# Performance work log

Measured on AMD Instinct MI355X. Metric: run time of the kernel, lower is better.

Reference implementation:

```python
import jax, jax.numpy as jnp
import numpy as np

NB, NC = 100000, 10000   # buildings, communities
EB, EC = 400000, 80000   # edges
BD, CD = 64, 32          # feature dims


def _glorot(key, shape):
    fan_in = shape[-2] if len(shape) > 1 else shape[0]
    return jax.random.normal(key, shape, jnp.float32) * (1.0 / np.sqrt(fan_in))


def setup_inputs() -> dict:
    key = jax.random.key(0)
    ks = iter(jax.random.split(key, 40))
    inp = {}
    inp['building_features'] = jax.random.normal(next(ks), (NB, BD), jnp.float32)
    inp['community_features'] = jax.random.normal(next(ks), (NC, CD), jnp.float32)
    inp['building_edge_index'] = jax.random.randint(next(ks), (2, EB), 0, NB, jnp.int32)
    inp['community_edge_index'] = jax.random.randint(next(ks), (2, EC), 0, NC, jnp.int32)
    inp['building_to_comm_mapping'] = jax.random.randint(next(ks), (NB,), 0, NC, jnp.int32)
    inp['c1_wl'] = _glorot(next(ks), (CD, 512)); inp['c1_wr'] = _glorot(next(ks), (CD, 512))
    inp['c1_att'] = _glorot(next(ks), (8, 64)); inp['c1_b'] = jnp.zeros((512,), jnp.float32)
    inp['c2_wl'] = _glorot(next(ks), (512, 128)); inp['c2_wr'] = _glorot(next(ks), (512, 128))
    inp['c2_att'] = _glorot(next(ks), (4, 32)); inp['c2_b'] = jnp.zeros((128,), jnp.float32)
    # feature attention: 8 heads of MLP (64+128)->128->2
    inp['fa_w1'] = _glorot(next(ks), (8, BD + 128, 128)); inp['fa_b1'] = jnp.zeros((8, 128), jnp.float32)
    inp['fa_w2'] = _glorot(next(ks), (8, 128, 2)); inp['fa_b2'] = jnp.zeros((8, 2), jnp.float32)
    inp['b1_wl'] = _glorot(next(ks), (BD + 128, 512)); inp['b1_wr'] = _glorot(next(ks), (BD + 128, 512))
    inp['b1_att'] = _glorot(next(ks), (8, 64)); inp['b1_b'] = jnp.zeros((512,), jnp.float32)
    inp['b2_wl'] = _glorot(next(ks), (512, 128)); inp['b2_wr'] = _glorot(next(ks), (512, 128))
    inp['b2_att'] = _glorot(next(ks), (4, 32)); inp['b2_b'] = jnp.zeros((128,), jnp.float32)
    inp['b3_wl'] = _glorot(next(ks), (128, 2)); inp['b3_wr'] = _glorot(next(ks), (128, 2))
    inp['b3_att'] = _glorot(next(ks), (1, 2)); inp['b3_b'] = jnp.zeros((2,), jnp.float32)
    return inp


def gatv2(x, src, dst, wl, wr, att, b, heads, out_dim, concat=True):
    """PyG GATv2Conv (eval mode, self-loops already appended to src/dst)."""
    n = x.shape[0]
    xl = (x @ wl).reshape(n, heads, out_dim)  # source transform
    xr = (x @ wr).reshape(n, heads, out_dim)  # target transform
    e = jax.nn.leaky_relu(xl[src] + xr[dst], 0.2)          # [E,H,D]
    logits = jnp.einsum('ehd,hd->eh', e, att)              # [E,H]
    m = jax.ops.segment_max(logits, dst, num_segments=n)   # stable softmax per target
    p = jnp.exp(logits - m[dst])
    denom = jax.ops.segment_sum(p, dst, num_segments=n)
    alpha = p / denom[dst]
    agg = jax.ops.segment_sum(alpha[:, :, None] * xl[src], dst, num_segments=n)
    agg = agg.reshape(n, heads * out_dim) if concat else agg.mean(axis=1)
    return agg + b


def _with_self_loops(edge_index, n):
    loops = jnp.arange(n, dtype=edge_index.dtype)
    return (jnp.concatenate([edge_index[0], loops]), jnp.concatenate([edge_index[1], loops]))


def _forward(building_features, community_features,
             c1_wl, c1_wr, c1_att, c1_b, c2_wl, c2_wr, c2_att, c2_b,
             fa_w1, fa_b1, fa_w2, fa_b2,
             b1_wl, b1_wr, b1_att, b1_b, b2_wl, b2_wr, b2_att, b2_b,
             b3_wl, b3_wr, b3_att, b3_b,
             building_edge_index, community_edge_index, building_to_comm_mapping):
    csrc, cdst = _with_self_loops(community_edge_index, NC)
    bsrc, bdst = _with_self_loops(building_edge_index, NB)
    # community GNN (dropout is identity in eval)
    cx = jax.nn.relu(gatv2(community_features, csrc, cdst, c1_wl, c1_wr, c1_att, c1_b, 8, 64))
    cx = jax.nn.relu(gatv2(cx, csrc, cdst, c2_wl, c2_wr, c2_att, c2_b, 4, 32))  # [NC,128]
    bcf = cx[building_to_comm_mapping]                                          # [NB,128]
    # multi-head feature attention fusion (vectorized over 8 heads)
    combined = jnp.concatenate([building_features, bcf], axis=1)                # [NB,192]
    h = jax.nn.relu(jnp.einsum('nf,hfk->nhk', combined, fa_w1) + fa_b1)         # [NB,8,128]
    w = jax.nn.softmax(jnp.einsum('nhk,hko->nho', h, fa_w2) + fa_b2, axis=-1)   # [NB,8,2]
    wmean = w.mean(axis=1)                                                      # mean over heads == mean of weighted copies
    fused = jnp.concatenate([building_features * wmean[:, 0:1], bcf * wmean[:, 1:2]], axis=1)
    # building GNN (single batched graph == Batch.from_data_list over all communities)
    x = jax.nn.relu(gatv2(fused, bsrc, bdst, b1_wl, b1_wr, b1_att, b1_b, 8, 64))
    x = jax.nn.relu(gatv2(x, bsrc, bdst, b2_wl, b2_wr, b2_att, b2_b, 4, 32))
    x = gatv2(x, bsrc, bdst, b3_wl, b3_wr, b3_att, b3_b, 1, 2)                   # [NB,2]
    return jax.nn.log_softmax(x, axis=1)


def reference(building_features, community_features,
              c1_wl, c1_wr, c1_att, c1_b, c2_wl, c2_wr, c2_att, c2_b,
              fa_w1, fa_b1, fa_w2, fa_b2,
              b1_wl, b1_wr, b1_att, b1_b, b2_wl, b2_wr, b2_att, b2_b,
              b3_wl, b3_wr, b3_att, b3_b,
              building_edge_index, community_edge_index, building_to_comm_mapping):
    return _forward(building_features, community_features,
                    c1_wl, c1_wr, c1_att, c1_b, c2_wl, c2_wr, c2_att, c2_b,
                    fa_w1, fa_b1, fa_w2, fa_b2,
                    b1_wl, b1_wr, b1_att, b1_b, b2_wl, b2_wr, b2_att, b2_b,
                    b3_wl, b3_wr, b3_att, b3_b,
                    building_edge_index, community_edge_index, building_to_comm_mapping)
```

## Files before the change

kernel.cpp:

```cpp
#include <hip/hip_runtime.h>

static constexpr int NBLD = 100000, NCOM = 10000, EBU = 400000, ECO = 80000;
static constexpr int EBT = EBU + NBLD;
static constexpr int ECT = ECO + NCOM;

typedef _Float16 f16;
typedef _Float16 f16x2 __attribute__((ext_vector_type(2)));
typedef _Float16 f16x8 __attribute__((ext_vector_type(8)));
typedef float f32x4 __attribute__((ext_vector_type(4)));

static constexpr size_t OFF_X1H  = 0;
static constexpr size_t OFF_CXL  = 0;
static constexpr size_t OFF_CXR  = 10240000;
static constexpr size_t OFF_CX1  = 20480000;
static constexpr size_t OFF_CX2L = 30720000;
static constexpr size_t OFF_CX2R = 33280000;
static constexpr size_t OFF_X2   = 0;
static constexpr size_t OFF_XLH  = 102400000;
static constexpr size_t OFF_XRH  = 128000000;
static constexpr size_t OFF_XL2  = 102400000;
static constexpr size_t OFF_XR2  = 128000000;
static constexpr size_t OFF_BF16 = 153600000;
static constexpr size_t OFF_CXF16= 166400000;
static constexpr size_t OFF_WM   = 168960000;
// ... 67 lines not shown
  int e = blockIdx.x * blockDim.x + threadIdx.x;
  if (e < EBT) {
    int dst = (e < EBU) ? bdst[e] : (e - EBU);
    atomicAdd(&bcnt[dst], 1);
  } else {
    int e2 = e - EBT;
    if (e2 >= ECT) return;
    int dst = (e2 < ECO) ? cdst[e2] : (e2 - ECO);
    atomicAdd(&ccnt[dst], 1);
  }
}

__global__ void k_scan1g(const int* __restrict__ bcnt, const int* __restrict__ ccnt,
                         int* __restrict__ boff, int* __restrict__ coff,
                         int* __restrict__ bsum, int* __restrict__ csum) {
  const int* cnt = blockIdx.y ? ccnt : bcnt;
  int* off = blockIdx.y ? coff : boff;
  int* sum = blockIdx.y ? csum : bsum;
  int N = blockIdx.y ? NCOM : NBLD;
  __shared__ int sh[256];
  int tid = threadIdx.x;
  int base = blockIdx.x * 2048 + tid * 8;
  int c[8]; int s = 0;
#pragma unroll
  for (int j = 0; j < 8; ++j) { int i = base + j; c[j] = (i < N) ? cnt[i] : 0; s += c[j]; }
  sh[tid] = s; __syncthreads();
  int own = s;
  for (int o = 1; o < 256; o <<= 1) {
    int v = (tid >= o) ? sh[tid - o] : 0; __syncthreads();
    sh[tid] += v; __syncthreads();
  }
  int ex = sh[tid] - own;
#pragma unroll
  for (int j = 0; j < 8; ++j) { int i = base + j; if (i < N) off[i] = ex; ex += c[j]; }
  if (tid == 255) sum[blockIdx.x] = sh[255];
}

__global__ void k_scan2g(const int* __restrict__ bsum, const int* __restrict__ csum,
                         int nb, int nc, int* __restrict__ bpre, int* __restrict__ cpre) {
  const int* sum = blockIdx.x ? csum : bsum;
  int n = blockIdx.x ? nc : nb;
  int* pre = blockIdx.x ? cpre : bpre;
  __shared__ int sh[256];
  int tid = threadIdx.x;
  int v0 = (tid < n) ? sum[tid] : 0;
  sh[tid] = v0; __syncthreads();
  for (int o = 1; o < 256; o <<= 1) {
    int v = (tid >= o) ? sh[tid - o] : 0; __syncthreads();
    sh[tid] += v; __syncthreads();
  }
  pre[tid] = sh[tid] - v0;
}

__global__ void k_scan3c(int* __restrict__ off, int N, const int* __restrict__ bpre, int Et,
                         int* __restrict__ cur) {
  int i = blockIdx.x * blockDim.x + threadIdx.x;
  if (i < N) {
    int v = off[i] + bpre[i >> 11];
    off[i] = v;
    cur[i] = v;
  }
  if (i == 0) off[N] = Et;
}

__global__ void k_scatter2(const int* __restrict__ bsrc, const int* __restrict__ bdst,
                           const int* __restrict__ csrc, const int* __restrict__ cdst,
                           int* __restrict__ bcur, int* __restrict__ ccur,
                           int* __restrict__ bout, int* __restrict__ cout) {
  int e = blockIdx.x * blockDim.x + threadIdx.x;
  if (e < EBT) {
    int s, d;
    if (e < EBU) { s = bsrc[e]; d = bdst[e]; } else { s = d = e - EBU; }
    bout[atomicAdd(&bcur[d], 1)] = s;
  } else {
    int e2 = e - EBT;
    if (e2 >= ECT) return;
    int s, d;
    if (e2 < ECO) { s = csrc[e2]; d = cdst[e2]; } else { s = d = e2 - ECO; }
    cout[atomicAdd(&ccur[d], 1)] = s;
  }
}


struct frag32 { f16x8 v0, v1; };

static __device__ inline frag32 loadA_lin(const f16* __restrict__ X, int lda,
                                          int k0, int tid, int bm, int M) {
  int row = tid >> 1, half = tid & 1;
  int grow = bm + row;
  frag32 r; r.v0 = (f16x8){}; r.v1 = (f16x8){};
  if (grow < M) {
    const f16* p = X + (size_t)grow * lda + k0 + half * 16;
    r.v0 = *(const f16x8*)(p);
    r.v1 = *(const f16x8*)(p + 8);
  }
  return r;
}

template<bool SCALE>
static __device__ inline frag32 loadA_fused(const f16* __restrict__ bf16h,
                                            const f16* __restrict__ cx16, int mrow,
                                            f16 s0, f16 s1, int k0, int tid, int grow, int M) {
  int half = tid & 1;
  int gc = k0 + half * 16;
  frag32 r; r.v0 = (f16x8){}; r.v1 = (f16x8){};
  if (grow < M) {
    const f16* src; f16 s;
    if (gc < 64) { src = bf16h + (size_t)grow * 64 + gc; s = s0; }
    else         { src = cx16 + (size_t)mrow * 128 + (gc - 64); s = s1; }
    r.v0 = *(const f16x8*)(src);
    r.v1 = *(const f16x8*)(src + 8);
    if (SCALE) {
#pragma unroll
      for (int j = 0; j < 8; ++j) { r.v0[j] *= s; r.v1[j] *= s; }
    }
  }
  return r;
}

static __device__ inline frag32 loadB_T(const f16* __restrict__ WT, int ldk, int k0, int tid) {
  int col = tid >> 1, half = tid & 1;
  const f16* p = WT + (size_t)col * ldk + k0 + half * 16;
  frag32 r;
  r.v0 = *(const f16x8*)(p);
  r.v1 = *(const f16x8*)(p + 8);
  return r;
}

static __device__ inline frag32 loadB_Tpair(const f16* __restrict__ WLt, const f16* __restrict__ WRt,
                                            int ldk, int slab, int k0, int tid) {
  int col = tid >> 1, half = tid & 1;
  const f16* base = (col < 64) ? (WLt + (size_t)(slab + col) * ldk)
                               : (WRt + (size_t)(slab + col - 64) * ldk);
  const f16* p = base + k0 + half * 16;
  frag32 r;
  r.v0 = *(const f16x8*)(p);
  r.v1 = *(const f16x8*)(p + 8);
  return r;
}

static __device__ inline void writeFrag(f16 (*S)[40], frag32 f, int tid) {
  int row = tid >> 1, half = tid & 1;
  *(f16x8*)&S[row][half * 16]     = f.v0;
  *(f16x8*)&S[row][half * 16 + 8] = f.v1;
}

static __device__ inline void mma_tiles(const f16 (*As)[40], const f16 (*Bs)[40],
                                        f32x4 acc[4][4], int wm, int wn, int lane) {
  int rl = lane & 15;
  int kg = (lane >> 4) * 8;
  f16x8 a[4], b[4];
#pragma unroll
  for (int i = 0; i < 4; ++i) a[i] = *(const f16x8*)&As[wm * 64 + i * 16 + rl][kg];
#pragma unroll
  for (int j = 0; j < 4; ++j) b[j] = *(const f16x8*)&Bs[wn * 64 + j * 16 + rl][kg];
#pragma unroll
  for (int i = 0; i < 4; ++i)
#pragma unroll
    for (int j = 0; j < 4; ++j)
      acc[i][j] = __builtin_amdgcn_mfma_f32_16x16x32_f16(a[i], b[j], acc[i][j], 0, 0, 0);
}

template<int NCB>
__global__ __launch_bounds__(256) void k_mgemm_gen(
    const f16* __restrict__ A, int lda,
    const f16* __restrict__ WT, int K,
    f16* __restrict__ out0, f16* __restrict__ out1, int N0, int ldo, int M) {
  __shared__ f16 As[2][128][40];
  __shared__ f16 Bs[2][128][40];
  int tid = threadIdx.x;
  int ppx = gridDim.x / (8 * NCB);
  int xcd = blockIdx.x & 7;
  int j6 = blockIdx.x >> 3;
  int cb = j6 % NCB;
  int p = xcd * ppx + j6 / NCB;
  int bm = p * 128;
  if (bm >= M) return;
  int bn = cb * 128;
  int lane = tid & 63, w = tid >> 6, wm_ = w >> 1, wn = w & 1;
  f32x4 acc[4][4];
#pragma unroll
  for (int i = 0; i < 4; ++i)
#pragma unroll
    for (int j = 0; j < 4; ++j) acc[i][j] = (f32x4){0.f, 0.f, 0.f, 0.f};

  const f16* WTb = WT + (size_t)bn * K;
  int NT = K >> 5;
  frag32 a0 = loadA_lin(A, lda, 0, tid, bm, M);
  frag32 b0 = loadB_T(WTb, K, 0, tid);
  frag32 a1; a1.v0 = (f16x8){}; a1.v1 = (f16x8){};
  frag32 b1v = a1;
  if (NT > 1) { a1 = loadA_lin(A, lda, 32, tid, bm, M); b1v = loadB_T(WTb, K, 32, tid); }
  for (int t = 0; t < NT; t += 2) {
    writeFrag(As[0], a0, tid); writeFrag(Bs[0], b0, tid);
    bool two = (t + 1 < NT);
    if (two) { writeFrag(As[1], a1, tid); writeFrag(Bs[1], b1v, tid); }
    __syncthreads();
    if (t + 2 < NT) {
      a0 = loadA_lin(A, lda, (t + 2) * 32, tid, bm, M);
      b0 = loadB_T(WTb, K, (t + 2) * 32, tid);
      if (t + 3 < NT) {
        a1 = loadA_lin(A, lda, (t + 3) * 32, tid, bm, M);
        b1v = loadB_T(WTb, K, (t + 3) * 32, tid);
      }
    }
    mma_tiles(As[0], Bs[0], acc, wm_, wn, lane);
    if (two) mma_tiles(As[1], Bs[1], acc, wm_, wn, lane);
    __syncthreads();
  }
  int rbase = bm + wm_ * 64 + (lane >> 4) * 4;
  int cl = lane & 15;
#pragma unroll
  for (int mi = 0; mi < 4; ++mi)
#pragma unroll
    for (int ni = 0; ni < 4; ++ni) {
      int col = bn + wn * 64 + ni * 16 + cl;
      f16* o; int c;
      if (col < N0) { o = out0; c = col; } else { o = out1; c = col - N0; }
#pragma unroll
      for (int r = 0; r < 4; ++r) {
        int row = rbase + mi * 16 + r;
        if (row < M) o[(size_t)row * ldo + c] = (f16)acc[mi][ni][r];
      }
    }
}

__global__ __launch_bounds__(256) void k_mgemm_b1(
    const f16* __restrict__ bf16h, const f16* __restrict__ cx16,
    const int* __restrict__ map, const float* __restrict__ wmv,
    const f16* __restrict__ WLt, const f16* __restrict__ WRt, int slabBase,
    f16* __restrict__ outl, f16* __restrict__ outr, int M) {
  __shared__ f16 As[2][128][40];
  __shared__ f16 Bs[2][128][40];
  int tid = threadIdx.x;
  int ppx = gridDim.x >> 4;
  int xcd = blockIdx.x & 7;
  int j6 = blockIdx.x >> 3;
  int ch = j6 & 1;
  int p = xcd * ppx + (j6 >> 1);
  int bm = p * 128;
  if (bm >= M) return;
  int slab = slabBase + ch * 64;
  int colbase = ch * 64;
  int lane = tid & 63, w = tid >> 6, wm_ = w >> 1, wn = w & 1;
  f32x4 acc[4][4];
#pragma unroll
  for (int i = 0; i < 4; ++i)
#pragma unroll
    for (int j = 0; j < 4; ++j) acc[i][j] = (f32x4){0.f, 0.f, 0.f, 0.f};

  int arow = bm + (tid >> 1);
  int mrow = 0; f16 s0 = (f16)1.f, s1 = (f16)1.f;
  if (arow < M) {
    mrow = map[arow];
    s0 = (f16)wmv[(size_t)arow * 2];
    s1 = (f16)wmv[(size_t)arow * 2 + 1];
  }

  frag32 a0 = loadA_fused<true>(bf16h, cx16, mrow, s0, s1, 0, tid, arow, M);
  frag32 b0 = loadB_Tpair(WLt, WRt, 192, slab, 0, tid);
  frag32 a1 = loadA_fused<true>(bf16h, cx16, mrow, s0, s1, 32, tid, arow, M);
  frag32 b1v = loadB_Tpair(WLt, WRt, 192, slab, 32, tid);
  for (int t = 0; t < 6; t += 2) {
    writeFrag(As[0], a0, tid); writeFrag(Bs[0], b0, tid);
    writeFrag(As[1], a1, tid); writeFrag(Bs[1], b1v, tid);
    __syncthreads();
    if (t + 2 < 6) {
      a0 = loadA_fused<true>(bf16h, cx16, mrow, s0, s1, (t + 2) * 32, tid, arow, M);
      b0 = loadB_Tpair(WLt, WRt, 192, slab, (t + 2) * 32, tid);
      a1 = loadA_fused<true>(bf16h, cx16, mrow, s0, s1, (t + 3) * 32, tid, arow, M);
      b1v = loadB_Tpair(WLt, WRt, 192, slab, (t + 3) * 32, tid);
    }
    mma_tiles(As[0], Bs[0], acc, wm_, wn, lane);
    mma_tiles(As[1], Bs[1], acc, wm_, wn, lane);
    __syncthreads();
  }
  int rbase = bm + wm_ * 64 + (lane >> 4) * 4;
  int cl = lane & 15;
#pragma unroll
  for (int mi = 0; mi < 4; ++mi)
#pragma unroll
    for (int ni = 0; ni < 4; ++ni) {
      int col = wn * 64 + ni * 16 + cl;
      f16* o = (col < 64) ? outl : outr;
      int c = colbase + (col & 63);
#pragma unroll
      for (int r = 0; r < 4; ++r) {
        int row = rbase + mi * 16 + r;
        if (row < M) o[(size_t)row * 128 + c] = (f16)acc[mi][ni][r];
      }
    }
}

__global__ __launch_bounds__(256) void k_mgemm_fa(
    const f16* __restrict__ bf16h, const f16* __restrict__ cx16,
    const int* __restrict__ map,
    const f16* __restrict__ w1T, const float* __restrict__ b1,
    const float* __restrict__ w2, const float* __restrict__ b2,
    float* __restrict__ wmout, int M) {
  __shared__ f16 As[2][128][40];
  __shared__ f16 Bs[2][128][40];
  __shared__ float sred[128][4];
  int tid = threadIdx.x;
  int ppx = gridDim.x >> 6;
  int xcd = blockIdx.x & 7;
  int j6 = blockIdx.x >> 3;
  int p = xcd * ppx + (j6 >> 3);
  int h = j6 & 7;
  int bm = p * 128;
  if (bm >= M) return;
  int lane = tid & 63, w = tid >> 6, wm_ = w >> 1, wn = w & 1;
  f32x4 acc[4][4];
#pragma unroll
  for (int i = 0; i < 4; ++i)
#pragma unroll
    for (int j = 0; j < 4; ++j) acc[i][j] = (f32x4){0.f, 0.f, 0.f, 0.f};

  int arow = bm + (tid >> 1);
  int mrow = (arow < M) ? map[arow] : 0;
  const f16* WT = w1T + (size_t)h * 128 * 192;

  frag32 a0 = loadA_fused<false>(bf16h, cx16, mrow, (f16)1.f, (f16)1.f, 0, tid, arow, M);
  frag32 b0 = loadB_T(WT, 192, 0, tid);
  frag32 a1 = loadA_fused<false>(bf16h, cx16, mrow, (f16)1.f, (f16)1.f, 32, tid, arow, M);
  frag32 b1v = loadB_T(WT, 192, 32, tid);
  for (int t = 0; t < 6; t += 2) {
    writeFrag(As[0], a0, tid); writeFrag(Bs[0], b0, tid);
    writeFrag(As[1], a1, tid); writeFrag(Bs[1], b1v, tid);
    __syncthreads();
    if (t + 2 < 6) {
      a0 = loadA_fused<false>(bf16h, cx16, mrow, (f16)1.f, (f16)1.f, (t + 2) * 32, tid, arow, M);
      b0 = loadB_T(WT, 192, (t + 2) * 32, tid);
      a1 = loadA_fused<false>(bf16h, cx16, mrow, (f16)1.f, (f16)1.f, (t + 3) * 32, tid, arow, M);
      b1v = loadB_T(WT, 192, (t + 3) * 32, tid);
    }
    mma_tiles(As[0], Bs[0], acc, wm_, wn, lane);
    mma_tiles(As[1], Bs[1], acc, wm_, wn, lane);
    __syncthreads();
  }

  int cl = lane & 15;
#pragma unroll
  for (int mi = 0; mi < 4; ++mi) {
    float t0[4] = {0.f, 0.f, 0.f, 0.f}, t1[4] = {0.f, 0.f, 0.f, 0.f};
#pragma unroll
    for (int ni = 0; ni < 4; ++ni) {
      int col = wn * 64 + ni * 16 + cl;
      float b1c = b1[h * 128 + col];
      float w0c = w2[((size_t)h * 128 + col) * 2];
      float w1c = w2[((size_t)h * 128 + col) * 2 + 1];
#pragma unroll
      for (int r = 0; r < 4; ++r) {
        float hv = fmaxf(acc[mi][ni][r] + b1c, 0.f);
        t0[r] = fmaf(hv, w0c, t0[r]);
        t1[r] = fmaf(hv, w1c, t1[r]);
      }
    }
#pragma unroll
    for (int m = 1; m < 16; m <<= 1) {
#pragma unroll
      for (int r = 0; r < 4; ++r) { t0[r] += __shfl_xor(t0[r], m); t1[r] += __shfl_xor(t1[r], m); }
    }
    if (cl == 0) {
#pragma unroll
      for (int r = 0; r < 4; ++r) {
        int rib = wm_ * 64 + mi * 16 + (lane >> 4) * 4 + r;
        sred[rib][wn] = t0[r];
        sred[rib][2 + wn] = t1[r];
      }
    }
  }
  __syncthreads();
  if (tid < 128) {
    int grow = bm + tid;
    if (grow < M) {
      float l0 = sred[tid][0] + sred[tid][1] + b2[h * 2];
      float l1 = sred[tid][2] + sred[tid][3] + b2[h * 2 + 1];
      float mx = fmaxf(l0, l1);
      float e0 = __expf(l0 - mx), e1 = __expf(l1 - mx);
      float inv = 0.125f / (e0 + e1);
      atomicAdd(&wmout[(size_t)grow * 2], e0 * inv);
      atomicAdd(&wmout[(size_t)grow * 2 + 1], e1 * inv);
    }
  }
}

template<int V, int G, bool RELU, typename IT, typename OT>
__global__ __launch_bounds__(256) void k_convf(const IT* __restrict__ xl, const IT* __restrict__ xr,
                                               const float* __restrict__ attw, const float* __restrict__ bias,
                                               const int* __restrict__ off, const int* __restrict__ srcl,
                                               OT* __restrict__ outp, int N, int ldx, int ldo) {
  int n = (int)((blockIdx.x * (unsigned)blockDim.x + threadIdx.x) >> 6);
  if (n >= N) return;
  int lane = threadIdx.x & 63;
  int base = lane * V;
  float xr_r[V], att_r[V], acc[V];
#pragma unroll
  for (int j = 0; j < V; ++j) {
    xr_r[j] = (float)xr[(size_t)n * ldx + base + j];
    att_r[j] = attw[base + j];
    acc[j] = 0.f;
  }
  float mh = -INFINITY, lh = 0.f;
  int p0 = off[n], p1 = off[n + 1];
  for (int p = p0; p < p1; ++p) {
    int src = srcl[p];
    float xlv[V];
    if constexpr (V == 2 && sizeof(IT) == 2) {
      f16x2 t = *(const f16x2*)(&xl[(size_t)src * ldx + base]);
      xlv[0] = (float)t[0]; xlv[1] = (float)t[1];
    } else if constexpr (V == 8 && sizeof(IT) == 2) {
      f16x8 t = *(const f16x8*)(&xl[(size_t)src * ldx + base]);
#pragma unroll
      for (int j = 0; j < 8; ++j) xlv[j] = (float)t[j];
    } else {
#pragma unroll
      for (int j = 0; j < V; ++j) xlv[j] = (float)xl[(size_t)src * ldx + base + j];
    }
    float part = 0.f;
#pragma unroll
    for (int j = 0; j < V; ++j) {
      float t = xlv[j] + xr_r[j];
      t = t > 0.f ? t : 0.2f * t;
      part = fmaf(t, att_r[j], part);
    }
#pragma unroll
    for (int m = 1; m < G; m <<= 1) part += __shfl_xor(part, m);
    float mn = fmaxf(mh, part);
    float scl = __expf(mh - mn);
    float pe = __expf(part - mn);
    lh = lh * scl + pe;
#pragma unroll
    for (int j = 0; j < V; ++j) acc[j] = acc[j] * scl + pe * xlv[j];
    mh = mn;
  }
  float inv = 1.f / lh;
#pragma unroll
  for (int j = 0; j < V; ++j) {
    float v = fmaf(acc[j], inv, bias[base + j]);
    if (RELU) v = fmaxf(v, 0.f);
    outp[(size_t)n * ldo + base + j] = (OT)v;
  }
}

__global__ __launch_bounds__(256) void k_b3gemm(const float* __restrict__ x2, const float* __restrict__ wl,
                                                const float* __restrict__ wr,
                                                float* __restrict__ xl3, float* __restrict__ xr3, int NB) {
  int n = (int)((blockIdx.x * (unsigned)blockDim.x + threadIdx.x) >> 6);
  if (n >= NB) return;
  int lane = threadIdx.x & 63;
  float2 a = *(const float2*)(x2 + (size_t)n * 128 + lane * 2);
  float4 wlv = *(const float4*)(wl + lane * 4);
  float4 wrv = *(const float4*)(wr + lane * 4);
  float l0 = a.x * wlv.x + a.y * wlv.z;
  float l1 = a.x * wlv.y + a.y * wlv.w;
  float r0 = a.x * wrv.x + a.y * wrv.z;
  float r1 = a.x * wrv.y + a.y * wrv.w;
#pragma unroll
  for (int m = 1; m < 64; m <<= 1) {
    l0 += __shfl_xor(l0, m); l1 += __shfl_xor(l1, m);
    r0 += __shfl_xor(r0, m); r1 += __shfl_xor(r1, m);
  }
  if (lane == 0) {
    xl3[(size_t)n * 2] = l0; xl3[(size_t)n * 2 + 1] = l1;
    xr3[(size_t)n * 2] = r0; xr3[(size_t)n * 2 + 1] = r1;
  }
}

__global__ void k_conv3(const float* __restrict__ xl, const float* __restrict__ xr,
                        const float* __restrict__ att, const float* __restrict__ bias,
                        const int* __restrict__ off, const int* __restrict__ srcl,
                        float* __restrict__ out, int NB) {
  int n = blockIdx.x * blockDim.x + threadIdx.x;
  if (n >= NB) return;
  float a0 = att[0], a1 = att[1];
  float xr0 = xr[(size_t)n * 2], xr1 = xr[(size_t)n * 2 + 1];
  float mh = -INFINITY, lh = 0.f, c0 = 0.f, c1 = 0.f;
  int p0 = off[n], p1 = off[n + 1];
  for (int p = p0; p < p1; ++p) {
    int src = srcl[p];
    float sl0 = xl[(size_t)src * 2], sl1 = xl[(size_t)src * 2 + 1];
    float t0 = sl0 + xr0; t0 = t0 > 0.f ? t0 : 0.2f * t0;
    float t1 = sl1 + xr1; t1 = t1 > 0.f ? t1 : 0.2f * t1;
    float lg = t0 * a0 + t1 * a1;
    float mn = fmaxf(mh, lg);
    float scl = __expf(mh - mn);
    float pe = __expf(lg - mn);
    lh = lh * scl + pe;
    c0 = c0 * scl + pe * sl0;
    c1 = c1 * scl + pe * sl1;
    mh = mn;
  }
  float inv = 1.f / lh;
  float v0 = c0 * inv + bias[0];
  float v1 = c1 * inv + bias[1];
  float mx = fmaxf(v0, v1);
  float ls = mx + logf(__expf(v0 - mx) + __expf(v1 - mx));
  out[(size_t)n * 2] = v0 - ls;
  out[(size_t)n * 2 + 1] = v1 - ls;
}

static inline int cdiv(int a, int b) { return (a + b - 1) / b; }

extern "C" void kernel_launch(void* const* d_in, const int* in_sizes, int n_in,
                              void* d_out, int out_size, void* d_ws, size_t ws_size,
                              hipStream_t stream) {
  (void)in_sizes; (void)n_in; (void)out_size; (void)ws_size;
  const float* bfeat = (const float*)d_in[0];
  const float* cfeat = (const float*)d_in[1];
  const int* bei = (const int*)d_in[2];
  const int* cei = (const int*)d_in[3];
  const int* b2c = (const int*)d_in[4];
  const float* c1_wl = (const float*)d_in[5];
  const float* c1_wr = (const float*)d_in[6];
  const float* c1_att = (const float*)d_in[7];
  const float* c1_b = (const float*)d_in[8];
  const float* c2_wl = (const float*)d_in[9];
  const float* c2_wr = (const float*)d_in[10];
  const float* c2_att = (const float*)d_in[11];
  const float* c2_b = (const float*)d_in[12];
  const float* fa_w1 = (const float*)d_in[13];
  const float* fa_b1 = (const float*)d_in[14];
  const float* fa_w2 = (const float*)d_in[15];
  const float* fa_b2 = (const float*)d_in[16];
  const float* b1_wl = (const float*)d_in[17];
  const float* b1_wr = (const float*)d_in[18];
  const float* b1_att = (const float*)d_in[19];
  const float* b1_b = (const float*)d_in[20];
  const float* b2_wl = (const float*)d_in[21];
  const float* b2_wr = (const float*)d_in[22];
  const float* b2_att = (const float*)d_in[23];
  const float* b2_b = (const float*)d_in[24];
  const float* b3_wl = (const float*)d_in[25];
  const float* b3_wr = (const float*)d_in[26];
  const float* b3_att = (const float*)d_in[27];
  const float* b3_b = (const float*)d_in[28];
  char* ws = (char*)d_ws;
  float* out = (float*)d_out;

  const int* b_src_arr = bei;
  const int* b_dst_arr = bei + EBU;
  const int* c_src_arr = cei;
  const int* c_dst_arr = cei + ECO;

  f16*   X1H  = (f16*)(ws + OFF_X1H);
  float* X2   = (float*)(ws + OFF_X2);
  f16*   XLH  = (f16*)(ws + OFF_XLH);
  f16*   XRH  = (f16*)(ws + OFF_XRH);
  f16*   XL2  = (f16*)(ws + OFF_XL2);
  f16*   XR2  = (f16*)(ws + OFF_XR2);
  f16*   CXLh = (f16*)(ws + OFF_CXL);
  f16*   CXRh = (f16*)(ws + OFF_CXR);
  f16*   CX1h = (f16*)(ws + OFF_CX1);
  f16*   CX2Lh= (f16*)(ws + OFF_CX2L);
  f16*   CX2Rh= (f16*)(ws + OFF_CX2R);
  f16*   BF16 = (f16*)(ws + OFF_BF16);
  f16*   CXF16= (f16*)(ws + OFF_CXF16);
  float* WM   = (float*)(ws + OFF_WM);
  float* XL3  = (float*)(ws + OFF_XL3);
  float* XR3  = (float*)(ws + OFF_XR3);
  f16*   FAW  = (f16*)(ws + OFF_FAW);
  f16*   B1LT = (f16*)(ws + OFF_B1LT);
  f16*   B1RT = (f16*)(ws + OFF_B1RT);
  f16*   B2T  = (f16*)(ws + OFF_B2T);
  f16*   C1T  = (f16*)(ws + OFF_C1T);
  f16*   C2T  = (f16*)(ws + OFF_C2T);
  f16*   CF16 = (f16*)(ws + OFF_CF16);
  int* BOFF = (int*)(ws + OFF_BOFF);
  int* BCUR = (int*)(ws + OFF_BCUR);
  int* BSRC = (int*)(ws + OFF_BSRC);
  int* COFF = (int*)(ws + OFF_COFF);
  int* CCUR = (int*)(ws + OFF_CCUR);
  int* CSRC = (int*)(ws + OFF_CSRC);
  int* SC1  = (int*)(ws + OFF_SC1);
  int* SC2  = (int*)(ws + OFF_SC2);
  int* SC1C = (int*)(ws + OFF_SC1C);
  int* SC2C = (int*)(ws + OFF_SC2C);

  k_cvtall<<<dim3(cdiv(192 * 512, 256), 16), 256, 0, stream>>>(
      fa_w1, b1_wl, b1_wr, b2_wl, b2_wr, c1_wl, c1_wr, c2_wl, c2_wr,
      FAW, B1LT, B1RT, B2T, C1T, C2T);
  k_cvt4<<<cdiv(NBLD * 16, 256), 256, 0, stream>>>(bfeat, BF16, NBLD * 16);
  k_cvt4<<<cdiv(NCOM * 8, 256), 256, 0, stream>>>(cfeat, CF16, NCOM * 8);

  k_zero2<<<cdiv(NBLD + NCOM, 256), 256, 0, stream>>>(BCUR, NBLD, CCUR, NCOM);
  k_count2<<<cdiv(EBT + ECT, 256), 256, 0, stream>>>(b_dst_arr, c_dst_arr, BCUR, CCUR);
  k_scan1g<<<dim3(cdiv(NBLD, 2048), 2), 256, 0, stream>>>(BCUR, CCUR, BOFF, COFF, SC1, SC1C);
  k_scan2g<<<2, 256, 0, stream>>>(SC1, SC1C, cdiv(NBLD, 2048), cdiv(NCOM, 2048), SC2, SC2C);
  k_scan3c<<<cdiv(NBLD, 256), 256, 0, stream>>>(BOFF, NBLD, SC2, EBT, BCUR);
  k_scan3c<<<cdiv(NCOM, 256), 256, 0, stream>>>(COFF, NCOM, SC2C, ECT, CCUR);
  k_scatter2<<<cdiv(EBT + ECT, 256), 256, 0, stream>>>(
      b_src_arr, b_dst_arr, c_src_arr, c_dst_arr, BCUR, CCUR, BSRC, CSRC);

  {
    int pC = cdiv(cdiv(NCOM, 128), 8);
    k_mgemm_gen<8><<<8 * pC * 8, 256, 0, stream>>>(
        CF16, 32, C1T, 32, CXLh, CXRh, 512, 512, NCOM);
    k_convf<8, 8, true, f16, f16><<<cdiv(NCOM, 4), 256, 0, stream>>>(
        CXLh, CXRh, c1_att, c1_b, COFF, CSRC, CX1h, NCOM, 512, 512);
    k_mgemm_gen<2><<<8 * pC * 2, 256, 0, stream>>>(
        CX1h, 512, C2T, 512, CX2Lh, CX2Rh, 128, 128, NCOM);
    k_convf<2, 16, true, f16, f16><<<cdiv(NCOM, 4), 256, 0, stream>>>(
        CX2Lh, CX2Rh, c2_att, c2_b, COFF, CSRC, CXF16, NCOM, 128, 128);
  }

  k_zerof<<<cdiv(NBLD * 2, 256), 256, 0, stream>>>(WM, NBLD * 2);
  {
    int panels = cdiv(NBLD, 128);
    int ppx = cdiv(panels, 8);
    k_mgemm_fa<<<64 * ppx, 256, 0, stream>>>(
        BF16, CXF16, b2c, FAW, fa_b1, fa_w2, fa_b2, WM, NBLD);
  }

  {
    int pB = cdiv(cdiv(NBLD, 128), 8);
    for (int cp = 0; cp < 4; ++cp) {
      k_mgemm_b1<<<16 * pB, 256, 0, stream>>>(
          BF16, CXF16, b2c, WM, B1LT, B1RT, cp * 128, XLH, XRH, NBLD);
      k_convf<2, 32, true, f16, f16><<<cdiv(NBLD, 4), 256, 0, stream>>>(
          XLH, XRH, b1_att + cp * 128, b1_b + cp * 128, BOFF, BSRC, X1H + cp * 128, NBLD, 128, 512);
    }
    k_mgemm_gen<2><<<8 * pB * 2, 256, 0, stream>>>(
        X1H, 512, B2T, 512, XL2, XR2, 128, 128, NBLD);
  }

  k_convf<2, 16, true, f16, float><<<cdiv(NBLD, 4), 256, 0, stream>>>(
      XL2, XR2, b2_att, b2_b, BOFF, BSRC, X2, NBLD, 128, 128);

  k_b3gemm<<<cdiv(NBLD, 4), 256, 0, stream>>>(X2, b3_wl, b3_wr, XL3, XR3, NBLD);
  k_conv3<<<cdiv(NBLD, 256), 256, 0, stream>>>(XL3, XR3, b3_att, b3_b, BOFF, BSRC, out, NBLD);
}
```

Baseline: 942.4 us.

## Enlarge GEMM M-tile to 256 rows and prefetch next neighbor row in aggregation

All MFMA GEMM kernels now process 256-row panels, with each thread loading a full 32-wide A row and each wave computing an 8x4 grid of 16x16 tiles. This halves the number of B-tile loads per output row and doubles MFMA work per sync. The GAT aggregation loops also software-prefetch the next source row's features so the gather load overlaps the current edge's softmax update. The larger tiles double accumulator registers and LDS use, which may lower occupancy and reduce the number of blocks launched for the small community graph.

```diff
diff --git a/kernel.cpp b/kernel.cpp
--- a/kernel.cpp
+++ b/kernel.cpp
@@ -173,37 +173,34 @@
 }
 
 
+struct frag64 { f16x8 v0, v1, v2, v3; };
 struct frag32 { f16x8 v0, v1; };
 
-static __device__ inline frag32 loadA_lin(const f16* __restrict__ X, int lda,
+static __device__ inline frag64 loadA_lin(const f16* __restrict__ X, int lda,
                                           int k0, int tid, int bm, int M) {
-  int row = tid >> 1, half = tid & 1;
-  int grow = bm + row;
-  frag32 r; r.v0 = (f16x8){}; r.v1 = (f16x8){};
+  int grow = bm + tid;
+  frag64 r; r.v0 = (f16x8){}; r.v1 = (f16x8){}; r.v2 = (f16x8){}; r.v3 = (f16x8){};
   if (grow < M) {
-    const f16* p = X + (size_t)grow * lda + k0 + half * 16;
-    r.v0 = *(const f16x8*)(p);
-    r.v1 = *(const f16x8*)(p + 8);
+    const f16x8* p = (const f16x8*)(X + (size_t)grow * lda + k0);
+    r.v0 = p[0]; r.v1 = p[1]; r.v2 = p[2]; r.v3 = p[3];
   }
   return r;
 }
 
 template<bool SCALE>
-static __device__ inline frag32 loadA_fused(const f16* __restrict__ bf16h,
+static __device__ inline frag64 loadA_fused(const f16* __restrict__ bf16h,
                                             const f16* __restrict__ cx16, int mrow,
                                             f16 s0, f16 s1, int k0, int tid, int grow, int M) {
-  int half = tid & 1;
-  int gc = k0 + half * 16;
-  frag32 r; r.v0 = (f16x8){}; r.v1 = (f16x8){};
+  frag64 r; r.v0 = (f16x8){}; r.v1 = (f16x8){}; r.v2 = (f16x8){}; r.v3 = (f16x8){};
   if (grow < M) {
     const f16* src; f16 s;
-    if (gc < 64) { src = bf16h + (size_t)grow * 64 + gc; s = s0; }
-    else         { src = cx16 + (size_t)mrow * 128 + (gc - 64); s = s1; }
-    r.v0 = *(const f16x8*)(src);
-    r.v1 = *(const f16x8*)(src + 8);
+    if (k0 < 64) { src = bf16h + (size_t)grow * 64 + k0; s = s0; }
+    else         { src = cx16 + (size_t)mrow * 128 + (k0 - 64); s = s1; }
+    const f16x8* p = (const f16x8*)src;
+    r.v0 = p[0]; r.v1 = p[1]; r.v2 = p[2]; r.v3 = p[3];
     if (SCALE) {
 #pragma unroll
-      for (int j = 0; j < 8; ++j) { r.v0[j] *= s; r.v1[j] *= s; }
+      for (int j = 0; j < 8; ++j) { r.v0[j] *= s; r.v1[j] *= s; r.v2[j] *= s; r.v3[j] *= s; }
     }
   }
   return r;
@@ -230,34 +227,46 @@
   return r;
 }
 
-static __device__ inline void writeFrag(f16 (*S)[40], frag32 f, int tid) {
-  int row = tid >> 1, half = tid & 1;
-  *(f16x8*)&S[row][half * 16]     = f.v0;
-  *(f16x8*)&S[row][half * 16 + 8] = f.v1;
+static __device__ inline void writeA(f16 (*S)[40], frag64 f, int tid) {
+  *(f16x8*)&S[tid][0]  = f.v0;
+  *(f16x8*)&S[tid][8]  = f.v1;
+  *(f16x8*)&S[tid][16] = f.v2;
+  *(f16x8*)&S[tid][24] = f.v3;
+}
+
+static __device__ inline void writeB(f16 (*S)[40], frag32 f, int tid) {
+  int col = tid >> 1, half = tid & 1;
+  *(f16x8*)&S[col][half * 16]     = f.v0;
+  *(f16x8*)&S[col][half * 16 + 8] = f.v1;
 }
 
 static __device__ inline void mma_tiles(const f16 (*As)[40], const f16 (*Bs)[40],
-                                        f32x4 acc[4][4], int wm, int wn, int lane) {
+                                        f32x4 acc[8][4], int wm, int wn, int lane) {
   int rl = lane & 15;
   int kg = (lane >> 4) * 8;
-  f16x8 a[4], b[4];
-#pragma unroll
-  for (int i = 0; i < 4; ++i) a[i] = *(const f16x8*)&As[wm * 64 + i * 16 + rl][kg];
+  f16x8 a[8], b[4];
+#pragma unroll
+  for (int i = 0; i < 8; ++i) a[i] = *(const f16x8*)&As[wm * 128 + i * 16 + rl][kg];
 #pragma unroll
   for (int j = 0; j < 4; ++j) b[j] = *(const f16x8*)&Bs[wn * 64 + j * 16 + rl][kg];
 #pragma unroll
-  for (int i = 0; i < 4; ++i)
+  for (int i = 0; i < 8; ++i)
 #pragma unroll
     for (int j = 0; j < 4; ++j)
       acc[i][j] = __builtin_amdgcn_mfma_f32_16x16x32_f16(a[i], b[j], acc[i][j], 0, 0, 0);
 }
+
+#define ACC_INIT(acc)                                     \
+  _Pragma("unroll") for (int i = 0; i < 8; ++i)           \
+  _Pragma("unroll") for (int j = 0; j < 4; ++j)           \
+      acc[i][j] = (f32x4){0.f, 0.f, 0.f, 0.f};
 
 template<int NCB>
 __global__ __launch_bounds__(256) void k_mgemm_gen(
     const f16* __restrict__ A, int lda,
     const f16* __restrict__ WT, int K,
     f16* __restrict__ out0, f16* __restrict__ out1, int N0, int ldo, int M) {
-  __shared__ f16 As[2][128][40];
+  __shared__ f16 As[2][256][40];
   __shared__ f16 Bs[2][128][40];
   int tid = threadIdx.x;
   int ppx = gridDim.x / (8 * NCB);
@@ -265,27 +274,23 @@
   int j6 = blockIdx.x >> 3;
   int cb = j6 % NCB;
   int p = xcd * ppx + j6 / NCB;
-  int bm = p * 128;
+  int bm = p * 256;
   if (bm >= M) return;
   int bn = cb * 128;
   int lane = tid & 63, w = tid >> 6, wm_ = w >> 1, wn = w & 1;
-  f32x4 acc[4][4];
-#pragma unroll
-  for (int i = 0; i < 4; ++i)
-#pragma unroll
-    for (int j = 0; j < 4; ++j) acc[i][j] = (f32x4){0.f, 0.f, 0.f, 0.f};
+  f32x4 acc[8][4];
+  ACC_INIT(acc)
 
   const f16* WTb = WT + (size_t)bn * K;
   int NT = K >> 5;
-  frag32 a0 = loadA_lin(A, lda, 0, tid, bm, M);
+  frag64 a0 = loadA_lin(A, lda, 0, tid, bm, M);
   frag32 b0 = loadB_T(WTb, K, 0, tid);
-  frag32 a1; a1.v0 = (f16x8){}; a1.v1 = (f16x8){};
-  frag32 b1v = a1;
+  frag64 a1; frag32 b1v;
   if (NT > 1) { a1 = loadA_lin(A, lda, 32, tid, bm, M); b1v = loadB_T(WTb, K, 32, tid); }
   for (int t = 0; t < NT; t += 2) {
-    writeFrag(As[0], a0, tid); writeFrag(Bs[0], b0, tid);
+    writeA(As[0], a0, tid); writeB(Bs[0], b0, tid);
     bool two = (t + 1 < NT);
-    if (two) { writeFrag(As[1], a1, tid); writeFrag(Bs[1], b1v, tid); }
+    if (two) { writeA(As[1], a1, tid); writeB(Bs[1], b1v, tid); }
     __syncthreads();
     if (t + 2 < NT) {
       a0 = loadA_lin(A, lda, (t + 2) * 32, tid, bm, M);
@@ -299,10 +304,10 @@
     if (two) mma_tiles(As[1], Bs[1], acc, wm_, wn, lane);
     __syncthreads();
   }
-  int rbase = bm + wm_ * 64 + (lane >> 4) * 4;
+  int rbase = bm + wm_ * 128 + (lane >> 4) * 4;
   int cl = lane & 15;
 #pragma unroll
-  for (int mi = 0; mi < 4; ++mi)
+  for (int mi = 0; mi < 8; ++mi)
 #pragma unroll
     for (int ni = 0; ni < 4; ++ni) {
       int col = bn + wn * 64 + ni * 16 + cl;
@@ -321,7 +326,7 @@
     const int* __restrict__ map, const float* __restrict__ wmv,
     const f16* __restrict__ WLt, const f16* __restrict__ WRt, int slabBase,
     f16* __restrict__ outl, f16* __restrict__ outr, int M) {
-  __shared__ f16 As[2][128][40];
+  __shared__ f16 As[2][256][40];
   __shared__ f16 Bs[2][128][40];
   int tid = threadIdx.x;
   int ppx = gridDim.x >> 4;
@@ -329,18 +334,15 @@
   int j6 = blockIdx.x >> 3;
   int ch = j6 & 1;
   int p = xcd * ppx + (j6 >> 1);
-  int bm = p * 128;
+  int bm = p * 256;
   if (bm >= M) return;
   int slab = slabBase + ch * 64;
   int colbase = ch * 64;
   int lane = tid & 63, w = tid >> 6, wm_ = w >> 1, wn = w & 1;
-  f32x4 acc[4][4];
-#pragma unroll
-  for (int i = 0; i < 4; ++i)
-#pragma unroll
-    for (int j = 0; j < 4; ++j) acc[i][j] = (f32x4){0.f, 0.f, 0.f, 0.f};
-
-  int arow = bm + (tid >> 1);
+  f32x4 acc[8][4];
+  ACC_INIT(acc)
+
+  int arow = bm + tid;
   int mrow = 0; f16 s0 = (f16)1.f, s1 = (f16)1.f;
   if (arow < M) {
     mrow = map[arow];
@@ -348,13 +350,13 @@
     s1 = (f16)wmv[(size_t)arow * 2 + 1];
   }
 
-  frag32 a0 = loadA_fused<true>(bf16h, cx16, mrow, s0, s1, 0, tid, arow, M);
+  frag64 a0 = loadA_fused<true>(bf16h, cx16, mrow, s0, s1, 0, tid, arow, M);
   frag32 b0 = loadB_Tpair(WLt, WRt, 192, slab, 0, tid);
-  frag32 a1 = loadA_fused<true>(bf16h, cx16, mrow, s0, s1, 32, tid, arow, M);
+  frag64 a1 = loadA_fused<true>(bf16h, cx16, mrow, s0, s1, 32, tid, arow, M);
   frag32 b1v = loadB_Tpair(WLt, WRt, 192, slab, 32, tid);
   for (int t = 0; t < 6; t += 2) {
-    writeFrag(As[0], a0, tid); writeFrag(Bs[0], b0, tid);
-    writeFrag(As[1], a1, tid); writeFrag(Bs[1], b1v, tid);
+    writeA(As[0], a0, tid); writeB(Bs[0], b0, tid);
+    writeA(As[1], a1, tid); writeB(Bs[1], b1v, tid);
     __syncthreads();
     if (t + 2 < 6) {
       a0 = loadA_fused<true>(bf16h, cx16, mrow, s0, s1, (t + 2) * 32, tid, arow, M);
@@ -366,10 +368,10 @@
     mma_tiles(As[1], Bs[1], acc, wm_, wn, lane);
     __syncthreads();
   }
-  int rbase = bm + wm_ * 64 + (lane >> 4) * 4;
+  int rbase = bm + wm_ * 128 + (lane >> 4) * 4;
   int cl = lane & 15;
 #pragma unroll
-  for (int mi = 0; mi < 4; ++mi)
+  for (int mi = 0; mi < 8; ++mi)
 #pragma unroll
     for (int ni = 0; ni < 4; ++ni) {
       int col = wn * 64 + ni * 16 + cl;
@@ -389,35 +391,32 @@
     const f16* __restrict__ w1T, const float* __restrict__ b1,
     const float* __restrict__ w2, const float* __restrict__ b2,
     float* __restrict__ wmout, int M) {
-  __shared__ f16 As[2][128][40];
+  __shared__ f16 As[2][256][40];
   __shared__ f16 Bs[2][128][40];
-  __shared__ float sred[128][4];
+  __shared__ float sred[256][4];
   int tid = threadIdx.x;
   int ppx = gridDim.x >> 6;
   int xcd = blockIdx.x & 7;
   int j6 = blockIdx.x >> 3;
   int p = xcd * ppx + (j6 >> 3);
   int h = j6 & 7;
-  int bm = p * 128;
+  int bm = p * 256;
   if (bm >= M) return;
   int lane = tid & 63, w = tid >> 6, wm_ = w >> 1, wn = w & 1;
-  f32x4 acc[4][4];
-#pragma unroll
-  for (int i = 0; i < 4; ++i)
-#pragma unroll
-    for (int j = 0; j < 4; ++j) acc[i][j] = (f32x4){0.f, 0.f, 0.f, 0.f};
-
-  int arow = bm + (tid >> 1);
+  f32x4 acc[8][4];
+  ACC_INIT(acc)
+
+  int arow = bm + tid;
   int mrow = (arow < M) ? map[arow] : 0;
   const f16* WT = w1T + (size_t)h * 128 * 192;
 
-  frag32 a0 = loadA_fused<false>(bf16h, cx16, mrow, (f16)1.f, (f16)1.f, 0, tid, arow, M);
+  frag64 a0 = loadA_fused<false>(bf16h, cx16, mrow, (f16)1.f, (f16)1.f, 0, tid, arow, M);
   frag32 b0 = loadB_T(WT, 192, 0, tid);
-  frag32 a1 = loadA_fused<false>(bf16h, cx16, mrow, (f16)1.f, (f16)1.f, 32, tid, arow, M);
+  frag64 a1 = loadA_fused<false>(bf16h, cx16, mrow, (f16)1.f, (f16)1.f, 32, tid, arow, M);
   frag32 b1v = loadB_T(WT, 192, 32, tid);
   for (int t = 0; t < 6; t += 2) {
-    writeFrag(As[0], a0, tid); writeFrag(Bs[0], b0, tid);
-    writeFrag(As[1], a1, tid); writeFrag(Bs[1], b1v, tid);
+    writeA(As[0], a0, tid); writeB(Bs[0], b0, tid);
+    writeA(As[1], a1, tid); writeB(Bs[1], b1v, tid);
     __syncthreads();
     if (t + 2 < 6) {
       a0 = loadA_fused<false>(bf16h, cx16, mrow, (f16)1.f, (f16)1.f, (t + 2) * 32, tid, arow, M);
@@ -432,7 +431,7 @@
 
   int cl = lane & 15;
 #pragma unroll
-  for (int mi = 0; mi < 4; ++mi) {
+  for (int mi = 0; mi < 8; ++mi) {
     float t0[4] = {0.f, 0.f, 0.f, 0.f}, t1[4] = {0.f, 0.f, 0.f, 0.f};
 #pragma unroll
     for (int ni = 0; ni < 4; ++ni) {
@@ -455,14 +454,14 @@
     if (cl == 0) {
 #pragma unroll
       for (int r = 0; r < 4; ++r) {
-        int rib = wm_ * 64 + mi * 16 + (lane >> 4) * 4 + r;
+        int rib = wm_ * 128 + mi * 16 + (lane >> 4) * 4 + r;
         sred[rib][wn] = t0[r];
         sred[rib][2 + wn] = t1[r];
       }
     }
   }
   __syncthreads();
-  if (tid < 128) {
+  {
     int grow = bm + tid;
     if (grow < M) {
       float l0 = sred[tid][0] + sred[tid][1] + b2[h * 2];
@@ -494,20 +493,27 @@
   }
   float mh = -INFINITY, lh = 0.f;
   int p0 = off[n], p1 = off[n + 1];
+
+  f16 rawn[V];
+  auto ldrow = [&](int src, f16* dst) {
+    if constexpr (V == 2 && sizeof(IT) == 2) {
+      *(f16x2*)dst = *(const f16x2*)(&xl[(size_t)src * ldx + base]);
+    } else if constexpr (V == 8 && sizeof(IT) == 2) {
+      *(f16x8*)dst = *(const f16x8*)(&xl[(size_t)src * ldx + base]);
+    } else {
+#pragma unroll
+      for (int j = 0; j < V; ++j) dst[j] = (f16)xl[(size_t)src * ldx + base + j];
+    }
+  };
+  if (p0 < p1) ldrow(srcl[p0], rawn);
   for (int p = p0; p < p1; ++p) {
-    int src = srcl[p];
+    f16 raw[V];
+#pragma unroll
+    for (int j = 0; j < V; ++j) raw[j] = rawn[j];
+    if (p + 1 < p1) ldrow(srcl[p + 1], rawn);
     float xlv[V];
-    if constexpr (V == 2 && sizeof(IT) == 2) {
-      f16x2 t = *(const f16x2*)(&xl[(size_t)src * ldx + base]);
-      xlv[0] = (float)t[0]; xlv[1] = (float)t[1];
-    } else if constexpr (V == 8 && sizeof(IT) == 2) {
-      f16x8 t = *(const f16x8*)(&xl[(size_t)src * ldx + base]);
-#pragma unroll
-      for (int j = 0; j < 8; ++j) xlv[j] = (float)t[j];
-    } else {
-#pragma unroll
-      for (int j = 0; j < V; ++j) xlv[j] = (float)xl[(size_t)src * ldx + base + j];
-    }
+#pragma unroll
+    for (int j = 0; j < V; ++j) xlv[j] = (float)raw[j];
     float part = 0.f;
 #pragma unroll
     for (int j = 0; j < V; ++j) {
@@ -568,9 +574,11 @@
   float xr0 = xr[(size_t)n * 2], xr1 = xr[(size_t)n * 2 + 1];
   float mh = -INFINITY, lh = 0.f, c0 = 0.f, c1 = 0.f;
   int p0 = off[n], p1 = off[n + 1];
+  float2 rawn = make_float2(0.f, 0.f);
+  if (p0 < p1) rawn = *(const float2*)(xl + (size_t)srcl[p0] * 2);
   for (int p = p0; p < p1; ++p) {
-    int src = srcl[p];
-    float sl0 = xl[(size_t)src * 2], sl1 = xl[(size_t)src * 2 + 1];
+    float sl0 = rawn.x, sl1 = rawn.y;
+    if (p + 1 < p1) rawn = *(const float2*)(xl + (size_t)srcl[p + 1] * 2);
     float t0 = sl0 + xr0; t0 = t0 > 0.f ? t0 : 0.2f * t0;
     float t1 = sl1 + xr1; t1 = t1 > 0.f ? t1 : 0.2f * t1;
     float lg = t0 * a0 + t1 * a1;
@@ -684,7 +692,7 @@
       b_src_arr, b_dst_arr, c_src_arr, c_dst_arr, BCUR, CCUR, BSRC, CSRC);
 
   {
-    int pC = cdiv(cdiv(NCOM, 128), 8);
+    int pC = cdiv(cdiv(NCOM, 256), 8);
     k_mgemm_gen<8><<<8 * pC * 8, 256, 0, stream>>>(
         CF16, 32, C1T, 32, CXLh, CXRh, 512, 512, NCOM);
     k_convf<8, 8, true, f16, f16><<<cdiv(NCOM, 4), 256, 0, stream>>>(
@@ -697,14 +705,14 @@
 
   k_zerof<<<cdiv(NBLD * 2, 256), 256, 0, stream>>>(WM, NBLD * 2);
   {
-    int panels = cdiv(NBLD, 128);
+    int panels = cdiv(NBLD, 256);
     int ppx = cdiv(panels, 8);
     k_mgemm_fa<<<64 * ppx, 256, 0, stream>>>(
         BF16, CXF16, b2c, FAW, fa_b1, fa_w2, fa_b2, WM, NBLD);
   }
 
   {
-    int pB = cdiv(cdiv(NBLD, 128), 8);
+    int pB = cdiv(cdiv(NBLD, 256), 8);
     for (int cp = 0; cp < 4; ++cp) {
       k_mgemm_b1<<<16 * pB, 256, 0, stream>>>(
           BF16, CXF16, b2c, WM, B1LT, B1RT, cp * 128, XLH, XRH, NBLD);
```

New measurement: 1.134 ms. 1.2x slower.

## Load GEMM weights directly from global into registers and prefetch gather rows

Applied to the files above, without the earlier changes.

The MFMA GEMM kernels stop staging the weight operand in shared memory. Each lane now reads its B fragments straight from global memory, which removes the shared-memory writes and reads for B and halves LDS use. The GATv2 aggregation loops software-prefetch the next neighbour's source row while the current edge is processed, to hide gather latency. In exchange, B reads become per-lane strided global loads (likely cached, since the weights are small). The prefetch path converts float inputs to f16, which can cost precision.

```diff
diff --git a/kernel.cpp b/kernel.cpp
--- a/kernel.cpp
+++ b/kernel.cpp
@@ -209,42 +209,22 @@
   return r;
 }
 
-static __device__ inline frag32 loadB_T(const f16* __restrict__ WT, int ldk, int k0, int tid) {
-  int col = tid >> 1, half = tid & 1;
-  const f16* p = WT + (size_t)col * ldk + k0 + half * 16;
-  frag32 r;
-  r.v0 = *(const f16x8*)(p);
-  r.v1 = *(const f16x8*)(p + 8);
-  return r;
-}
-
-static __device__ inline frag32 loadB_Tpair(const f16* __restrict__ WLt, const f16* __restrict__ WRt,
-                                            int ldk, int slab, int k0, int tid) {
-  int col = tid >> 1, half = tid & 1;
-  const f16* base = (col < 64) ? (WLt + (size_t)(slab + col) * ldk)
-                               : (WRt + (size_t)(slab + col - 64) * ldk);
-  const f16* p = base + k0 + half * 16;
-  frag32 r;
-  r.v0 = *(const f16x8*)(p);
-  r.v1 = *(const f16x8*)(p + 8);
-  return r;
-}
-
-static __device__ inline void writeFrag(f16 (*S)[40], frag32 f, int tid) {
+static __device__ inline void writeA(f16 (*S)[40], frag32 f, int tid) {
   int row = tid >> 1, half = tid & 1;
   *(f16x8*)&S[row][half * 16]     = f.v0;
   *(f16x8*)&S[row][half * 16 + 8] = f.v1;
 }
 
-static __device__ inline void mma_tiles(const f16 (*As)[40], const f16 (*Bs)[40],
-                                        f32x4 acc[4][4], int wm, int wn, int lane) {
+static __device__ inline void mma_direct(const f16 (*As)[40], const f16* const bb[4],
+                                         int kofs, f32x4 acc[4][4], int wm, int lane) {
   int rl = lane & 15;
   int kg = (lane >> 4) * 8;
-  f16x8 a[4], b[4];
+  f16x8 b[4];
+#pragma unroll
+  for (int j = 0; j < 4; ++j) b[j] = *(const f16x8*)(bb[j] + kofs + kg);
+  f16x8 a[4];
 #pragma unroll
   for (int i = 0; i < 4; ++i) a[i] = *(const f16x8*)&As[wm * 64 + i * 16 + rl][kg];
-#pragma unroll
-  for (int j = 0; j < 4; ++j) b[j] = *(const f16x8*)&Bs[wn * 64 + j * 16 + rl][kg];
 #pragma unroll
   for (int i = 0; i < 4; ++i)
 #pragma unroll
@@ -258,7 +238,6 @@
     const f16* __restrict__ WT, int K,
     f16* __restrict__ out0, f16* __restrict__ out1, int N0, int ldo, int M) {
   __shared__ f16 As[2][128][40];
-  __shared__ f16 Bs[2][128][40];
   int tid = threadIdx.x;
   int ppx = gridDim.x / (8 * NCB);
   int xcd = blockIdx.x & 7;
@@ -275,28 +254,29 @@
 #pragma unroll
     for (int j = 0; j < 4; ++j) acc[i][j] = (f32x4){0.f, 0.f, 0.f, 0.f};
 
-  const f16* WTb = WT + (size_t)bn * K;
+  int rl = lane & 15;
+  const f16* bb[4];
+#pragma unroll
+  for (int j = 0; j < 4; ++j) {
+    int col = bn + wn * 64 + j * 16 + rl;
+    bb[j] = WT + (size_t)col * K;
+  }
+
   int NT = K >> 5;
   frag32 a0 = loadA_lin(A, lda, 0, tid, bm, M);
-  frag32 b0 = loadB_T(WTb, K, 0, tid);
   frag32 a1; a1.v0 = (f16x8){}; a1.v1 = (f16x8){};
-  frag32 b1v = a1;
-  if (NT > 1) { a1 = loadA_lin(A, lda, 32, tid, bm, M); b1v = loadB_T(WTb, K, 32, tid); }
+  if (NT > 1) a1 = loadA_lin(A, lda, 32, tid, bm, M);
   for (int t = 0; t < NT; t += 2) {
-    writeFrag(As[0], a0, tid); writeFrag(Bs[0], b0, tid);
+    writeA(As[0], a0, tid);
     bool two = (t + 1 < NT);
-    if (two) { writeFrag(As[1], a1, tid); writeFrag(Bs[1], b1v, tid); }
+    if (two) writeA(As[1], a1, tid);
     __syncthreads();
     if (t + 2 < NT) {
       a0 = loadA_lin(A, lda, (t + 2) * 32, tid, bm, M);
-      b0 = loadB_T(WTb, K, (t + 2) * 32, tid);
-      if (t + 3 < NT) {
-        a1 = loadA_lin(A, lda, (t + 3) * 32, tid, bm, M);
-        b1v = loadB_T(WTb, K, (t + 3) * 32, tid);
-      }
-    }
-    mma_tiles(As[0], Bs[0], acc, wm_, wn, lane);
-    if (two) mma_tiles(As[1], Bs[1], acc, wm_, wn, lane);
+      if (t + 3 < NT) a1 = loadA_lin(A, lda, (t + 3) * 32, tid, bm, M);
+    }
+    mma_direct(As[0], bb, t * 32, acc, wm_, lane);
+    if (two) mma_direct(As[1], bb, (t + 1) * 32, acc, wm_, lane);
     __syncthreads();
   }
   int rbase = bm + wm_ * 64 + (lane >> 4) * 4;
@@ -322,7 +302,6 @@
     const f16* __restrict__ WLt, const f16* __restrict__ WRt, int slabBase,
     f16* __restrict__ outl, f16* __restrict__ outr, int M) {
   __shared__ f16 As[2][128][40];
-  __shared__ f16 Bs[2][128][40];
   int tid = threadIdx.x;
   int ppx = gridDim.x >> 4;
   int xcd = blockIdx.x & 7;
@@ -348,22 +327,27 @@
     s1 = (f16)wmv[(size_t)arow * 2 + 1];
   }
 
+  int rl = lane & 15;
+  const f16* bb[4];
+#pragma unroll
+  for (int j = 0; j < 4; ++j) {
+    int col = wn * 64 + j * 16 + rl;
+    bb[j] = (col < 64) ? (WLt + (size_t)(slab + col) * 192)
+                       : (WRt + (size_t)(slab + col - 64) * 192);
+  }
+
   frag32 a0 = loadA_fused<true>(bf16h, cx16, mrow, s0, s1, 0, tid, arow, M);
-  frag32 b0 = loadB_Tpair(WLt, WRt, 192, slab, 0, tid);
   frag32 a1 = loadA_fused<true>(bf16h, cx16, mrow, s0, s1, 32, tid, arow, M);
-  frag32 b1v = loadB_Tpair(WLt, WRt, 192, slab, 32, tid);
   for (int t = 0; t < 6; t += 2) {
-    writeFrag(As[0], a0, tid); writeFrag(Bs[0], b0, tid);
-    writeFrag(As[1], a1, tid); writeFrag(Bs[1], b1v, tid);
+    writeA(As[0], a0, tid);
+    writeA(As[1], a1, tid);
     __syncthreads();
     if (t + 2 < 6) {
       a0 = loadA_fused<true>(bf16h, cx16, mrow, s0, s1, (t + 2) * 32, tid, arow, M);
-      b0 = loadB_Tpair(WLt, WRt, 192, slab, (t + 2) * 32, tid);
       a1 = loadA_fused<true>(bf16h, cx16, mrow, s0, s1, (t + 3) * 32, tid, arow, M);
-      b1v = loadB_Tpair(WLt, WRt, 192, slab, (t + 3) * 32, tid);
-    }
-    mma_tiles(As[0], Bs[0], acc, wm_, wn, lane);
-    mma_tiles(As[1], Bs[1], acc, wm_, wn, lane);
+    }
+    mma_direct(As[0], bb, t * 32, acc, wm_, lane);
+    mma_direct(As[1], bb, (t + 1) * 32, acc, wm_, lane);
     __syncthreads();
   }
   int rbase = bm + wm_ * 64 + (lane >> 4) * 4;
@@ -390,7 +374,6 @@
     const float* __restrict__ w2, const float* __restrict__ b2,
     float* __restrict__ wmout, int M) {
   __shared__ f16 As[2][128][40];
-  __shared__ f16 Bs[2][128][40];
   __shared__ float sred[128][4];
   int tid = threadIdx.x;
   int ppx = gridDim.x >> 6;
@@ -411,22 +394,26 @@
   int mrow = (arow < M) ? map[arow] : 0;
   const f16* WT = w1T + (size_t)h * 128 * 192;
 
+  int rl = lane & 15;
+  const f16* bb[4];
+#pragma unroll
+  for (int j = 0; j < 4; ++j) {
+    int col = wn * 64 + j * 16 + rl;
+    bb[j] = WT + (size_t)col * 192;
+  }
+
   frag32 a0 = loadA_fused<false>(bf16h, cx16, mrow, (f16)1.f, (f16)1.f, 0, tid, arow, M);
-  frag32 b0 = loadB_T(WT, 192, 0, tid);
   frag32 a1 = loadA_fused<false>(bf16h, cx16, mrow, (f16)1.f, (f16)1.f, 32, tid, arow, M);
-  frag32 b1v = loadB_T(WT, 192, 32, tid);
   for (int t = 0; t < 6; t += 2) {
-    writeFrag(As[0], a0, tid); writeFrag(Bs[0], b0, tid);
-    writeFrag(As[1], a1, tid); writeFrag(Bs[1], b1v, tid);
+    writeA(As[0], a0, tid);
+    writeA(As[1], a1, tid);
     __syncthreads();
     if (t + 2 < 6) {
       a0 = loadA_fused<false>(bf16h, cx16, mrow, (f16)1.f, (f16)1.f, (t + 2) * 32, tid, arow, M);
-      b0 = loadB_T(WT, 192, (t + 2) * 32, tid);
       a1 = loadA_fused<false>(bf16h, cx16, mrow, (f16)1.f, (f16)1.f, (t + 3) * 32, tid, arow, M);
-      b1v = loadB_T(WT, 192, (t + 3) * 32, tid);
-    }
-    mma_tiles(As[0], Bs[0], acc, wm_, wn, lane);
-    mma_tiles(As[1], Bs[1], acc, wm_, wn, lane);
+    }
+    mma_direct(As[0], bb, t * 32, acc, wm_, lane);
+    mma_direct(As[1], bb, (t + 1) * 32, acc, wm_, lane);
     __syncthreads();
   }
 
@@ -494,20 +481,27 @@
   }
   float mh = -INFINITY, lh = 0.f;
   int p0 = off[n], p1 = off[n + 1];
+
+  f16 rawn[V];
+  auto ldrow = [&](int src, f16* dst) {
+    if constexpr (V == 2 && sizeof(IT) == 2) {
+      *(f16x2*)dst = *(const f16x2*)(&xl[(size_t)src * ldx + base]);
+    } else if constexpr (V == 8 && sizeof(IT) == 2) {
+      *(f16x8*)dst = *(const f16x8*)(&xl[(size_t)src * ldx + base]);
+    } else {
+#pragma unroll
+      for (int j = 0; j < V; ++j) dst[j] = (f16)xl[(size_t)src * ldx + base + j];
+    }
+  };
+  if (p0 < p1) ldrow(srcl[p0], rawn);
   for (int p = p0; p < p1; ++p) {
-    int src = srcl[p];
+    f16 raw[V];
+#pragma unroll
+    for (int j = 0; j < V; ++j) raw[j] = rawn[j];
+    if (p + 1 < p1) ldrow(srcl[p + 1], rawn);
     float xlv[V];
-    if constexpr (V == 2 && sizeof(IT) == 2) {
-      f16x2 t = *(const f16x2*)(&xl[(size_t)src * ldx + base]);
-      xlv[0] = (float)t[0]; xlv[1] = (float)t[1];
-    } else if constexpr (V == 8 && sizeof(IT) == 2) {
-      f16x8 t = *(const f16x8*)(&xl[(size_t)src * ldx + base]);
-#pragma unroll
-      for (int j = 0; j < 8; ++j) xlv[j] = (float)t[j];
-    } else {
-#pragma unroll
-      for (int j = 0; j < V; ++j) xlv[j] = (float)xl[(size_t)src * ldx + base + j];
-    }
+#pragma unroll
+    for (int j = 0; j < V; ++j) xlv[j] = (float)raw[j];
     float part = 0.f;
 #pragma unroll
     for (int j = 0; j < V; ++j) {
@@ -568,9 +562,11 @@
   float xr0 = xr[(size_t)n * 2], xr1 = xr[(size_t)n * 2 + 1];
   float mh = -INFINITY, lh = 0.f, c0 = 0.f, c1 = 0.f;
   int p0 = off[n], p1 = off[n + 1];
+  float2 rawn = make_float2(0.f, 0.f);
+  if (p0 < p1) rawn = *(const float2*)(xl + (size_t)srcl[p0] * 2);
   for (int p = p0; p < p1; ++p) {
-    int src = srcl[p];
-    float sl0 = xl[(size_t)src * 2], sl1 = xl[(size_t)src * 2 + 1];
+    float sl0 = rawn.x, sl1 = rawn.y;
+    if (p + 1 < p1) rawn = *(const float2*)(xl + (size_t)srcl[p + 1] * 2);
     float t0 = sl0 + xr0; t0 = t0 > 0.f ? t0 : 0.2f * t0;
     float t1 = sl1 + xr1; t1 = t1 > 0.f ? t1 : 0.2f * t1;
     float lg = t0 * a0 + t1 * a1;
```

Result: slower. 1.041 ms (+10.4%).
